# Optimization experiments

Hardware: AMD Instinct MI355X
Metric: run time of the kernel (lower is better)

Reference implementation:

```python
import jax, jax.numpy as jnp
import numpy as np

N = 50000
E = 800000
IN_DIM = 3
HID = 128
OUT_DIM = 3
RED = 16


def setup_inputs() -> dict:
    key = jax.random.key(0)
    ks = jax.random.split(key, 20)
    s = lambda k, shp: jax.random.normal(k, shp, dtype=jnp.float32) * 0.05
    inp = {
        'x': jax.random.normal(ks[0], (N, IN_DIM), dtype=jnp.float32),
        'edge_index': jax.random.randint(ks[1], (2, E), 0, N, dtype=jnp.int32),
        'deg_inv_sqrt': jax.random.uniform(ks[2], (N,), dtype=jnp.float32),
        # GCN layer weights (torch Linear convention: [out, in])
        'W1': s(ks[3], (HID, IN_DIM)), 'b1': s(ks[4], (HID,)),
        'W2': s(ks[5], (HID, HID)),    'b2': s(ks[6], (HID,)),
        'W3': s(ks[7], (HID, HID)),    'b3': s(ks[8], (HID,)),
        # channel attention MLPs (no bias): C -> C//RED -> C
        'ca1_w1': s(ks[9],  (HID // RED, HID)), 'ca1_w2': s(ks[10], (HID, HID // RED)),
        'ca2_w1': s(ks[11], (HID // RED, HID)), 'ca2_w2': s(ks[12], (HID, HID // RED)),
        'ca3_w1': s(ks[13], (HID // RED, HID)), 'ca3_w2': s(ks[14], (HID, HID // RED)),
        # output head
        'Wout': s(ks[15], (OUT_DIM, HID)), 'bout': s(ks[16], (OUT_DIM,)),
    }
    return inp


def _gcn(x, row, col, dis, W, b):
    # gather source features, normalize by deg_inv_sqrt[row]*deg_inv_sqrt[col], scatter-add to target
    norm = (dis[row] * dis[col])[:, None]          # [E,1]
    msg = x[row] * norm                             # [E,C]
    agg = jax.ops.segment_sum(msg, col, num_segments=x.shape[0])  # [N,C]
    return jax.nn.elu(agg @ W.T + b)


def _channel_attn(x, w1, w2):
    # global avg/max pool over nodes -> [C]; shared MLP; sigmoid gate
    avg = jnp.mean(x, axis=0)
    mx = jnp.max(x, axis=0)
    mlp = lambda v: jax.nn.relu(v @ w1.T) @ w2.T
    att = jax.nn.sigmoid(mlp(avg) + mlp(mx))        # [C]
    return x * att


def reference(x, edge_index, deg_inv_sqrt, W1, b1, W2, b2, W3, b3,
              ca1_w1, ca1_w2, ca2_w1, ca2_w2, ca3_w1, ca3_w2, Wout, bout):
    row, col = edge_index[0], edge_index[1]
    h = _gcn(x, row, col, deg_inv_sqrt, W1, b1)
    h = _channel_attn(h, ca1_w1, ca1_w2)
    h = _gcn(h, row, col, deg_inv_sqrt, W2, b2)
    h = _channel_attn(h, ca2_w1, ca2_w2)
    h = _gcn(h, row, col, deg_inv_sqrt, W3, b3)
    h = _channel_attn(h, ca3_w1, ca3_w2)
    return h @ Wout.T + bout
```

## Files before the change

kernel.cpp:

```cpp
#include <hip/hip_runtime.h>

#define NN 50000
#define NE 800000
#define NBD3 391
#define NBG 782
#define PMAX (NBG*128)
#define NRED 64

#define EC 4096
#define NBLKC 196
#define NBUCK 1563
#define LT (NBUCK*NBLKC)
#define NS1 300
#define DCAP 1024

typedef __attribute__((ext_vector_type(8))) short bf16x8;
typedef __attribute__((ext_vector_type(4))) float f32x4;

__device__ __forceinline__ float elu_f(float x){ return x > 0.f ? x : __expf(x) - 1.f; }

__device__ __forceinline__ ushort f2bf(float f){
    unsigned u = __float_as_uint(f);
    unsigned r = (u + 0x7FFFu + ((u >> 16) & 1u)) >> 16;
    return (ushort)r;
}
__device__ __forceinline__ float bf2f(short u){
    return __uint_as_float(((unsigned)(unsigned short)u) << 16);
}

__global__ __launch_bounds__(256) void k_bhist(const int* __restrict__ col, int* __restrict__ hist){
    __shared__ int h[NBUCK];
    int blk = blockIdx.x;
    for (int i = threadIdx.x; i < NBUCK; i += 256) h[i] = 0;
    __syncthreads();
    int base = blk * EC;
    #pragma unroll
    for (int i = 0; i < 16; ++i){
        int e = base + i*256 + threadIdx.x;
        if (e < NE) atomicAdd(&h[col[e] >> 5], 1);
    }
    __syncthreads();
    for (int i = threadIdx.x; i < NBUCK; i += 256) hist[i*NBLKC + blk] = h[i];
}

__global__ __launch_bounds__(256) void k_s1(const int* __restrict__ hist, int* __restrict__ bsum){
    __shared__ int red[256];
    int base = blockIdx.x*1024 + threadIdx.x;
    int s = 0;
    #pragma unroll
    for (int i = 0; i < 4; ++i){ int idx = base + i*256; if (idx < LT) s += hist[idx]; }
    red[threadIdx.x] = s;
    __syncthreads();
    for (int off = 128; off > 0; off >>= 1){
        if (threadIdx.x < off) red[threadIdx.x] += red[threadIdx.x + off];
        __syncthreads();
    }
    if (threadIdx.x == 0) bsum[blockIdx.x] = red[0];
}

__global__ __launch_bounds__(512) void k_s2(const int* __restrict__ bsum, int* __restrict__ boff){
    __shared__ int s[512];
    int t = threadIdx.x;
    int v = (t < NS1) ? bsum[t] : 0;
    s[t] = v;
    __syncthreads();
    for (int off = 1; off < 512; off <<= 1){
        int u = (t >= off) ? s[t - off] : 0;
        __syncthreads();
        s[t] += u;
        __syncthreads();
    }
    if (t < NS1) boff[t] = s[t] - v;
}

__global__ __launch_bounds__(256) void k_s3(const int* __restrict__ hist, const int* __restrict__ boff,
                                            int* __restrict__ scanned, int* __restrict__ bucketPtr){
    __shared__ int red[256];
    int blk = blockIdx.x, t = threadIdx.x;
    int base = blk*1024;
    int v[4]; int s = 0;
    #pragma unroll
    for (int i = 0; i < 4; ++i){
        int idx = base + t*4 + i;
        v[i] = (idx < LT) ? hist[idx] : 0;
        s += v[i];
    }
    red[t] = s;
    __syncthreads();
    for (int off = 1; off < 256; off <<= 1){
        int u = (t >= off) ? red[t - off] : 0;
        __syncthreads();
        red[t] += u;
        __syncthreads();
    }
    int run = boff[blk] + red[t] - s;
    #pragma unroll
    for (int i = 0; i < 4; ++i){
        int idx = base + t*4 + i;
        if (idx < LT){
            scanned[idx] = run;
            if (idx % NBLKC == 0) bucketPtr[idx / NBLKC] = run;
            run += v[i];
        }
    }
    if (blk == 0 && t == 0) bucketPtr[NBUCK] = NE;
}

__global__ __launch_bounds__(256) void k_csort(const int* __restrict__ row, const int* __restrict__ col,
                                               const int* __restrict__ scanned, int2* __restrict__ edgeS){
    __shared__ int curs[NBUCK];
    int blk = blockIdx.x;
    for (int i = threadIdx.x; i < NBUCK; i += 256) curs[i] = scanned[i*NBLKC + blk];
    __syncthreads();
    int base = blk * EC;
    #pragma unroll
    for (int i = 0; i < 16; ++i){
        int e = base + i*256 + threadIdx.x;
        if (e < NE){
            int r = row[e], c = col[e];
            int pos = atomicAdd(&curs[c >> 5], 1);
            edgeS[pos] = make_int2(r, c);
        }
    }
}

__global__ __launch_bounds__(256) void k_dsort(const float* __restrict__ dis, const int* __restrict__ bucketPtr,
                                               int2* __restrict__ edge, int* __restrict__ rowptr){
    __shared__ int nodeCnt[32];
    __shared__ int nodeOff[33];
    __shared__ float disL[32];
    __shared__ int2 stage[DCAP];
    int b = blockIdx.x, t = threadIdx.x;
    int j0 = bucketPtr[b], j1 = bucketPtr[b+1], cnt = j1 - j0;
    if (t < 32){
        nodeCnt[t] = 0;
        int c = b*32 + t;
        disL[t] = (c < NN) ? dis[c] : 0.f;
    }
    __syncthreads();
    int er[8], ec[8], rk[8]; int m = 0;
    for (int j = t; j < cnt && m < 8; j += 256){
        int2 e = edge[j0 + j];
        int cl = e.y & 31;
        er[m] = e.x; ec[m] = e.y;
        rk[m] = atomicAdd(&nodeCnt[cl], 1);
        ++m;
    }
    __syncthreads();
    if (t == 0){
        int run = 0;
        #pragma unroll
        for (int i = 0; i < 32; ++i){ nodeOff[i] = run; run += nodeCnt[i]; }
        nodeOff[32] = run;
    }
    __syncthreads();
    if (t < 32){
        int c = b*32 + t;
        if (c < NN) rowptr[c] = j0 + nodeOff[t];
    }
    if (b == 0 && t == 0) rowptr[NN] = NE;
    bool staged = (cnt <= DCAP);
    for (int i = 0; i < m; ++i){
        int r = er[i], cl = ec[i] & 31;
        float nm = dis[r] * disL[cl];
        int pos = nodeOff[cl] + rk[i];
        int2 rec = make_int2(r, __float_as_int(nm));
        if (staged) stage[pos] = rec;
        else        edge[j0 + pos] = rec;
    }
    __syncthreads();
    if (staged)
        for (int j = t; j < cnt; j += 256) edge[j0 + j] = stage[j];
}

__global__ void k_gather3(const float* __restrict__ x, const int* __restrict__ rowptr,
                          const int2* __restrict__ edge, float* __restrict__ agg){
    int n = blockIdx.x * blockDim.x + threadIdx.x;
    if (n >= NN) return;
    int j0 = rowptr[n], j1 = rowptr[n + 1];
    float a0 = 0.f, a1 = 0.f, a2 = 0.f;
    for (int j = j0; j < j1; ++j){
        int2 e = edge[j];
        int r = e.x; float w = __int_as_float(e.y);
        a0 = fmaf(x[r*3+0], w, a0);
        a1 = fmaf(x[r*3+1], w, a1);
        a2 = fmaf(x[r*3+2], w, a2);
    }
    agg[n*3+0] = a0; agg[n*3+1] = a1; agg[n*3+2] = a2;
}

__global__ __launch_bounds__(128) void k_dense3p(const float* __restrict__ agg, const float* __restrict__ W,
                          const float* __restrict__ b, ushort* __restrict__ h, float* __restrict__ part){
    int c = threadIdx.x;
    int n0 = blockIdx.x * 128;
    int n1 = min(n0 + 128, NN);
    float w0 = W[c*3+0], w1 = W[c*3+1], w2 = W[c*3+2], bb = b[c];
    float s = 0.f, m = -3.4e38f;
    for (int n = n0; n < n1; ++n){
        float v = fmaf(agg[n*3+0], w0, fmaf(agg[n*3+1], w1, fmaf(agg[n*3+2], w2, bb)));
        v = elu_f(v);
        h[(size_t)n*128 + c] = f2bf(v);
        s += v; m = fmaxf(m, v);
    }
    part[blockIdx.x*128 + c] = s;
    part[PMAX + blockIdx.x*128 + c] = m;
}

__global__ __launch_bounds__(256) void k_attn_pre(const float* __restrict__ part, int nblk,
                                                  float* __restrict__ part2){
    __shared__ float sS[2][128], sM[2][128];
    int c = threadIdx.x & 127, g = threadIdx.x >> 7;
    float s = 0.f, m = -3.4e38f;
    for (int b = blockIdx.x*2 + g; b < nblk; b += NRED*2){
        s += part[b*128 + c];
        m = fmaxf(m, part[PMAX + b*128 + c]);
    }
    sS[g][c] = s; sM[g][c] = m;
    __syncthreads();
    if (g == 0){
        part2[blockIdx.x*128 + c] = sS[0][c] + sS[1][c];
        part2[NRED*128 + blockIdx.x*128 + c] = fmaxf(sM[0][c], sM[1][c]);
    }
}

__global__ __launch_bounds__(512) void k_attn(const float* __restrict__ part2,
                       const float* __restrict__ w1, const float* __restrict__ w2,
                       const float* __restrict__ Wsrc, void* __restrict__ Wdst, int mode){
    __shared__ float sAll[4][128], mAll[4][128];
    __shared__ float avg[128], mx[128], ha[8], hm[8], attL[128];
    int c = threadIdx.x & 127, g = threadIdx.x >> 7;
    float s = 0.f, m = -3.4e38f;
    #pragma unroll
    for (int b = 0; b < NRED/4; ++b){
        int r = b*4 + g;
        s += part2[r*128 + c];
        m = fmaxf(m, part2[NRED*128 + r*128 + c]);
    }
    sAll[g][c] = s; mAll[g][c] = m;
    __syncthreads();
    if (g == 0){
        s = sAll[0][c] + sAll[1][c] + sAll[2][c] + sAll[3][c];
        m = fmaxf(fmaxf(mAll[0][c], mAll[1][c]), fmaxf(mAll[2][c], mAll[3][c]));
        avg[c] = s / (float)NN;
        mx[c] = m;
    }
    __syncthreads();
    if (threadIdx.x < 8){
        int cc = threadIdx.x;
        float sa = 0.f, sm = 0.f;
        for (int k = 0; k < 128; ++k){
            float w = w1[cc*128 + k];
            sa += avg[k]*w; sm += mx[k]*w;
        }
        ha[cc] = fmaxf(sa, 0.f); hm[cc] = fmaxf(sm, 0.f);
    }
    __syncthreads();
    if (threadIdx.x < 128){
        float oa = 0.f, om = 0.f;
        for (int j = 0; j < 8; ++j){
            float w = w2[c*8 + j];
            oa += ha[j]*w; om += hm[j]*w;
        }
        attL[c] = 1.f / (1.f + __expf(-(oa + om)));
    }
    __syncthreads();
    if (mode == 0){
        ushort* wd = (ushort*)Wdst;
        for (int i = threadIdx.x; i < 16384; i += 512)
            wd[i] = f2bf(Wsrc[i] * attL[i & 127]);
    } else {
        float* wd = (float*)Wdst;
        if (threadIdx.x < 384)
            wd[threadIdx.x] = Wsrc[threadIdx.x] * attL[threadIdx.x & 127];
    }
}

__global__ __launch_bounds__(256) void k_gg(const ushort* __restrict__ h,
                        const int* __restrict__ rowptr, const int2* __restrict__ edge,
                        const ushort* __restrict__ Wb, const float* __restrict__ b,
                        ushort* __restrict__ hout, float* __restrict__ part){
    __shared__ ushort At[64*128];
    __shared__ float poolS[4][128], poolM[4][128];
    int tid = threadIdx.x;
    int n0b = blockIdx.x * 64;

    {
        int node = tid >> 2;
        int q = tid & 3;
        int n = n0b + node;
        float acc[32];
        #pragma unroll
        for (int i = 0; i < 32; ++i) acc[i] = 0.f;
        if (n < NN){
            int j0 = rowptr[n], j1 = rowptr[n + 1];
            const ushort* hq = h + q*32;
            int j = j0;
            for (; j + 1 < j1; j += 2){
                int2 e0 = edge[j], e1 = edge[j+1];
                const ushort* r0 = hq + (size_t)e0.x*128;
                const ushort* r1 = hq + (size_t)e1.x*128;
                bf16x8 v00 = *(const bf16x8*)(r0);
                bf16x8 v01 = *(const bf16x8*)(r0 + 8);
                bf16x8 v02 = *(const bf16x8*)(r0 + 16);
                bf16x8 v03 = *(const bf16x8*)(r0 + 24);
                bf16x8 v10 = *(const bf16x8*)(r1);
                bf16x8 v11 = *(const bf16x8*)(r1 + 8);
                bf16x8 v12 = *(const bf16x8*)(r1 + 16);
                bf16x8 v13 = *(const bf16x8*)(r1 + 24);
                float w0 = __int_as_float(e0.y), w1 = __int_as_float(e1.y);
                #pragma unroll
                for (int cc = 0; cc < 8; ++cc){
                    acc[cc]    = fmaf(bf2f(v00[cc]), w0, acc[cc]);
                    acc[8+cc]  = fmaf(bf2f(v01[cc]), w0, acc[8+cc]);
                    acc[16+cc] = fmaf(bf2f(v02[cc]), w0, acc[16+cc]);
                    acc[24+cc] = fmaf(bf2f(v03[cc]), w0, acc[24+cc]);
                    acc[cc]    = fmaf(bf2f(v10[cc]), w1, acc[cc]);
                    acc[8+cc]  = fmaf(bf2f(v11[cc]), w1, acc[8+cc]);
                    acc[16+cc] = fmaf(bf2f(v12[cc]), w1, acc[16+cc]);
                    acc[24+cc] = fmaf(bf2f(v13[cc]), w1, acc[24+cc]);
                }
            }
            if (j < j1){
                int2 e0 = edge[j];
                const ushort* r0 = hq + (size_t)e0.x*128;
                bf16x8 v00 = *(const bf16x8*)(r0);
                bf16x8 v01 = *(const bf16x8*)(r0 + 8);
                bf16x8 v02 = *(const bf16x8*)(r0 + 16);
                bf16x8 v03 = *(const bf16x8*)(r0 + 24);
                float w0 = __int_as_float(e0.y);
                #pragma unroll
                for (int cc = 0; cc < 8; ++cc){
                    acc[cc]    = fmaf(bf2f(v00[cc]), w0, acc[cc]);
                    acc[8+cc]  = fmaf(bf2f(v01[cc]), w0, acc[8+cc]);
                    acc[16+cc] = fmaf(bf2f(v02[cc]), w0, acc[16+cc]);
                    acc[24+cc] = fmaf(bf2f(v03[cc]), w0, acc[24+cc]);
                }
            }
        }
        #pragma unroll
        for (int k = 0; k < 4; ++k){
            bf16x8 o;
            #pragma unroll
            for (int cc = 0; cc < 8; ++cc) o[cc] = (short)f2bf(acc[k*8 + cc]);
            int s = q*4 + k;
            *(bf16x8*)((char*)At + node*256 + ((s ^ (node & 7)) << 4)) = o;
        }
    }
    __syncthreads();

    int wave = tid >> 6, l = tid & 63;
    int lr = l & 15, lk = l >> 4;
    int r = wave*16 + lr;
    bf16x8 a[4];
    #pragma unroll
    for (int kb = 0; kb < 4; ++kb){
        int s = kb*4 + lk;
        a[kb] = *(const bf16x8*)((char*)At + r*256 + ((s ^ (r & 7)) << 4));
    }
    int n0 = n0b + wave*16;
    float s_part[8], m_part[8];
    const ushort* wbase = Wb + (size_t)lr * 128 + lk * 8;
    #pragma unroll
    for (int t = 0; t < 8; ++t){
        int j0 = t * 16;
        float bias = b[j0 + lr];
        f32x4 acc = {bias, bias, bias, bias};
        const ushort* wrow = wbase + (size_t)j0 * 128;
        #pragma unroll
        for (int kb = 0; kb < 4; ++kb){
            bf16x8 bf = *(const bf16x8*)(wrow + kb * 32);
            acc = __builtin_amdgcn_mfma_f32_16x16x32_bf16(a[kb], bf, acc, 0, 0, 0);
        }
        float s = 0.f, m = -3.4e38f;
        #pragma unroll
        for (int rr = 0; rr < 4; ++rr){
            int n = n0 + lk * 4 + rr;
            float v = elu_f(acc[rr]);
            if (n < NN){
                hout[(size_t)n * 128 + j0 + lr] = f2bf(v);
                s += v; m = fmaxf(m, v);
            }
        }
        s += __shfl_xor(s, 16); s += __shfl_xor(s, 32);
        m = fmaxf(m, __shfl_xor(m, 16)); m = fmaxf(m, __shfl_xor(m, 32));
        s_part[t] = s; m_part[t] = m;
    }
    if (lk == 0){
        #pragma unroll
        for (int t = 0; t < 8; ++t){
            poolS[wave][t * 16 + lr] = s_part[t];
            poolM[wave][t * 16 + lr] = m_part[t];
        }
    }
    __syncthreads();
    if (tid < 128){
        float S = poolS[0][tid] + poolS[1][tid] + poolS[2][tid] + poolS[3][tid];
        float M = fmaxf(fmaxf(poolM[0][tid], poolM[1][tid]), fmaxf(poolM[2][tid], poolM[3][tid]));
        part[blockIdx.x * 128 + tid] = S;
        part[PMAX + blockIdx.x * 128 + tid] = M;
    }
}

__global__ __launch_bounds__(256) void k_out(const ushort* __restrict__ h,
                      const float* __restrict__ WoS, const float* __restrict__ bo,
                      float* __restrict__ out){
    int n = blockIdx.x * blockDim.x + threadIdx.x;
    if (n >= NN) return;
    float acc0 = bo[0], acc1 = bo[1], acc2 = bo[2];
    const bf16x8* hv = (const bf16x8*)(h + (size_t)n*128);
    #pragma unroll
    for (int i = 0; i < 16; ++i){
        bf16x8 v = hv[i];
        #pragma unroll
        for (int c = 0; c < 8; ++c){
            int cc = i*8 + c;
            float hv_f = bf2f(v[c]);
            acc0 = fmaf(hv_f, WoS[cc],        acc0);
            acc1 = fmaf(hv_f, WoS[128 + cc],  acc1);
            acc2 = fmaf(hv_f, WoS[256 + cc],  acc2);
        }
    }
    out[n*3+0] = acc0; out[n*3+1] = acc1; out[n*3+2] = acc2;
}

extern "C" void kernel_launch(void* const* d_in, const int* in_sizes, int n_in,
                              void* d_out, int out_size, void* d_ws, size_t ws_size,
                              hipStream_t stream) {
    const float* x    = (const float*)d_in[0];
    const int*   ei   = (const int*)d_in[1];
    const int*   row  = ei;
    const int*   col  = ei + NE;
    const float* dis  = (const float*)d_in[2];
    const float* W1   = (const float*)d_in[3];
    const float* b1   = (const float*)d_in[4];
    const float* W2   = (const float*)d_in[5];
    const float* b2   = (const float*)d_in[6];
    const float* W3   = (const float*)d_in[7];
    const float* b3   = (const float*)d_in[8];
    const float* ca1w1= (const float*)d_in[9];
    const float* ca1w2= (const float*)d_in[10];
    const float* ca2w1= (const float*)d_in[11];
    const float* ca2w2= (const float*)d_in[12];
    const float* ca3w1= (const float*)d_in[13];
    const float* ca3w2= (const float*)d_in[14];
    const float* Wout = (const float*)d_in[15];
    const float* bout = (const float*)d_in[16];
    float* out = (float*)d_out;

    ushort* hB    = (ushort*)d_ws;
    ushort* hC    = hB + (size_t)NN*128;
    float*  agg3  = (float*)(hC + (size_t)NN*128);
    float*  part  = agg3 + (size_t)NN*3;
    float*  part2 = part + (size_t)2*PMAX;
    ushort* Wb2   = (ushort*)(part2 + 2*NRED*128);
    ushort* Wb3   = Wb2 + 16384;
    float*  WoutS = (float*)(Wb3 + 16384);
    int2*   edge  = (int2*)(WoutS + 384);
    int*    rowptr= (int*)(edge + NE);
    int*    hist  = rowptr + NN + 1;
    int*    scanned = hist + LT;
    int*    bucketPtr = scanned + LT;
    int*    bsum  = bucketPtr + NBUCK + 1;
    int*    boff  = bsum + NS1;

    k_bhist<<<NBLKC, 256, 0, stream>>>(col, hist);
    k_s1<<<NS1, 256, 0, stream>>>(hist, bsum);
    k_s2<<<1, 512, 0, stream>>>(bsum, boff);
    k_s3<<<NS1, 256, 0, stream>>>(hist, boff, scanned, bucketPtr);
    k_csort<<<NBLKC, 256, 0, stream>>>(row, col, scanned, edge);
    k_dsort<<<NBUCK, 256, 0, stream>>>(dis, bucketPtr, edge, rowptr);

    k_gather3<<<(NN+255)/256, 256, 0, stream>>>(x, rowptr, edge, agg3);
    k_dense3p<<<NBD3, 128, 0, stream>>>(agg3, W1, b1, hB, part);
    k_attn_pre<<<NRED, 256, 0, stream>>>(part, NBD3, part2);
    k_attn<<<1, 512, 0, stream>>>(part2, ca1w1, ca1w2, W2, (void*)Wb2, 0);

    k_gg<<<NBG, 256, 0, stream>>>(hB, rowptr, edge, Wb2, b2, hC, part);
    k_attn_pre<<<NRED, 256, 0, stream>>>(part, NBG, part2);
    k_attn<<<1, 512, 0, stream>>>(part2, ca2w1, ca2w2, W3, (void*)Wb3, 0);

    k_gg<<<NBG, 256, 0, stream>>>(hC, rowptr, edge, Wb3, b3, hB, part);
    k_attn_pre<<<NRED, 256, 0, stream>>>(part, NBG, part2);
    k_attn<<<1, 512, 0, stream>>>(part2, ca3w1, ca3w2, Wout, (void*)WoutS, 1);

    k_out<<<(NN+255)/256, 256, 0, stream>>>(hB, WoutS, bout, out);
}
```

Measured before the change: 220.2 us.

## Split fused gather-GEMM across 512 threads with 8 lanes per node

```diff
diff --git a/kernel.cpp b/kernel.cpp
--- a/kernel.cpp
+++ b/kernel.cpp
@@ -275,94 +275,89 @@
     }
 }
 
-__global__ __launch_bounds__(256) void k_gg(const ushort* __restrict__ h,
+__global__ __launch_bounds__(512) void k_gg(const ushort* __restrict__ h,
                         const int* __restrict__ rowptr, const int2* __restrict__ edge,
                         const ushort* __restrict__ Wb, const float* __restrict__ b,
                         ushort* __restrict__ hout, float* __restrict__ part){
     __shared__ ushort At[64*128];
-    __shared__ float poolS[4][128], poolM[4][128];
+    __shared__ float poolS[8][64], poolM[8][64];
     int tid = threadIdx.x;
     int n0b = blockIdx.x * 64;
 
     {
-        int node = tid >> 2;
-        int q = tid & 3;
+        int node = tid >> 3;
+        int l8 = tid & 7;
         int n = n0b + node;
-        float acc[32];
-        #pragma unroll
-        for (int i = 0; i < 32; ++i) acc[i] = 0.f;
+        float acc[16];
+        #pragma unroll
+        for (int i = 0; i < 16; ++i) acc[i] = 0.f;
         if (n < NN){
             int j0 = rowptr[n], j1 = rowptr[n + 1];
-            const ushort* hq = h + q*32;
+            const ushort* hq = h + l8*16;
             int j = j0;
-            for (; j + 1 < j1; j += 2){
-                int2 e0 = edge[j], e1 = edge[j+1];
+            for (; j + 3 < j1; j += 4){
+                int2 e0 = edge[j], e1 = edge[j+1], e2 = edge[j+2], e3 = edge[j+3];
                 const ushort* r0 = hq + (size_t)e0.x*128;
                 const ushort* r1 = hq + (size_t)e1.x*128;
-                bf16x8 v00 = *(const bf16x8*)(r0);
-                bf16x8 v01 = *(const bf16x8*)(r0 + 8);
-                bf16x8 v02 = *(const bf16x8*)(r0 + 16);
-                bf16x8 v03 = *(const bf16x8*)(r0 + 24);
-                bf16x8 v10 = *(const bf16x8*)(r1);
-                bf16x8 v11 = *(const bf16x8*)(r1 + 8);
-                bf16x8 v12 = *(const bf16x8*)(r1 + 16);
-                bf16x8 v13 = *(const bf16x8*)(r1 + 24);
+                const ushort* r2 = hq + (size_t)e2.x*128;
+                const ushort* r3 = hq + (size_t)e3.x*128;
+                bf16x8 v0a = *(const bf16x8*)(r0), v0b = *(const bf16x8*)(r0 + 8);
+                bf16x8 v1a = *(const bf16x8*)(r1), v1b = *(const bf16x8*)(r1 + 8);
+                bf16x8 v2a = *(const bf16x8*)(r2), v2b = *(const bf16x8*)(r2 + 8);
+                bf16x8 v3a = *(const bf16x8*)(r3), v3b = *(const bf16x8*)(r3 + 8);
                 float w0 = __int_as_float(e0.y), w1 = __int_as_float(e1.y);
+                float w2 = __int_as_float(e2.y), w3 = __int_as_float(e3.y);
                 #pragma unroll
                 for (int cc = 0; cc < 8; ++cc){
-                    acc[cc]    = fmaf(bf2f(v00[cc]), w0, acc[cc]);
-                    acc[8+cc]  = fmaf(bf2f(v01[cc]), w0, acc[8+cc]);
-                    acc[16+cc] = fmaf(bf2f(v02[cc]), w0, acc[16+cc]);
-                    acc[24+cc] = fmaf(bf2f(v03[cc]), w0, acc[24+cc]);
-                    acc[cc]    = fmaf(bf2f(v10[cc]), w1, acc[cc]);
-                    acc[8+cc]  = fmaf(bf2f(v11[cc]), w1, acc[8+cc]);
-                    acc[16+cc] = fmaf(bf2f(v12[cc]), w1, acc[16+cc]);
-                    acc[24+cc] = fmaf(bf2f(v13[cc]), w1, acc[24+cc]);
+                    acc[cc]   = fmaf(bf2f(v0a[cc]), w0, acc[cc]);
+                    acc[8+cc] = fmaf(bf2f(v0b[cc]), w0, acc[8+cc]);
+                    acc[cc]   = fmaf(bf2f(v1a[cc]), w1, acc[cc]);
+                    acc[8+cc] = fmaf(bf2f(v1b[cc]), w1, acc[8+cc]);
+                    acc[cc]   = fmaf(bf2f(v2a[cc]), w2, acc[cc]);
+                    acc[8+cc] = fmaf(bf2f(v2b[cc]), w2, acc[8+cc]);
+                    acc[cc]   = fmaf(bf2f(v3a[cc]), w3, acc[cc]);
+                    acc[8+cc] = fmaf(bf2f(v3b[cc]), w3, acc[8+cc]);
                 }
             }
-            if (j < j1){
+            for (; j < j1; ++j){
                 int2 e0 = edge[j];
                 const ushort* r0 = hq + (size_t)e0.x*128;
-                bf16x8 v00 = *(const bf16x8*)(r0);
-                bf16x8 v01 = *(const bf16x8*)(r0 + 8);
-                bf16x8 v02 = *(const bf16x8*)(r0 + 16);
-                bf16x8 v03 = *(const bf16x8*)(r0 + 24);
+                bf16x8 v0a = *(const bf16x8*)(r0), v0b = *(const bf16x8*)(r0 + 8);
                 float w0 = __int_as_float(e0.y);
                 #pragma unroll
                 for (int cc = 0; cc < 8; ++cc){
-                    acc[cc]    = fmaf(bf2f(v00[cc]), w0, acc[cc]);
-                    acc[8+cc]  = fmaf(bf2f(v01[cc]), w0, acc[8+cc]);
-                    acc[16+cc] = fmaf(bf2f(v02[cc]), w0, acc[16+cc]);
-                    acc[24+cc] = fmaf(bf2f(v03[cc]), w0, acc[24+cc]);
+                    acc[cc]   = fmaf(bf2f(v0a[cc]), w0, acc[cc]);
+                    acc[8+cc] = fmaf(bf2f(v0b[cc]), w0, acc[8+cc]);
                 }
             }
         }
         #pragma unroll
-        for (int k = 0; k < 4; ++k){
+        for (int k = 0; k < 2; ++k){
             bf16x8 o;
             #pragma unroll
             for (int cc = 0; cc < 8; ++cc) o[cc] = (short)f2bf(acc[k*8 + cc]);
-            int s = q*4 + k;
+            int s = l8*2 + k;
             *(bf16x8*)((char*)At + node*256 + ((s ^ (node & 7)) << 4)) = o;
         }
     }
     __syncthreads();
 
     int wave = tid >> 6, l = tid & 63;
+    int nt = wave >> 1, jh = wave & 1;
     int lr = l & 15, lk = l >> 4;
-    int r = wave*16 + lr;
+    int r = nt*16 + lr;
     bf16x8 a[4];
     #pragma unroll
     for (int kb = 0; kb < 4; ++kb){
         int s = kb*4 + lk;
         a[kb] = *(const bf16x8*)((char*)At + r*256 + ((s ^ (r & 7)) << 4));
     }
-    int n0 = n0b + wave*16;
-    float s_part[8], m_part[8];
+    int n0 = n0b + nt*16;
+    float s_part[4], m_part[4];
     const ushort* wbase = Wb + (size_t)lr * 128 + lk * 8;
     #pragma unroll
-    for (int t = 0; t < 8; ++t){
-        int j0 = t * 16;
+    for (int t = 0; t < 4; ++t){
+        int j0 = jh*64 + t*16;
         float bias = b[j0 + lr];
         f32x4 acc = {bias, bias, bias, bias};
         const ushort* wrow = wbase + (size_t)j0 * 128;
@@ -387,17 +382,19 @@
     }
     if (lk == 0){
         #pragma unroll
-        for (int t = 0; t < 8; ++t){
+        for (int t = 0; t < 4; ++t){
             poolS[wave][t * 16 + lr] = s_part[t];
             poolM[wave][t * 16 + lr] = m_part[t];
         }
     }
     __syncthreads();
     if (tid < 128){
-        float S = poolS[0][tid] + poolS[1][tid] + poolS[2][tid] + poolS[3][tid];
-        float M = fmaxf(fmaxf(poolM[0][tid], poolM[1][tid]), fmaxf(poolM[2][tid], poolM[3][tid]));
-        part[blockIdx.x * 128 + tid] = S;
-        part[PMAX + blockIdx.x * 128 + tid] = M;
+        int c = tid, j2 = c >> 6, lc = c & 63;
+        float S = poolS[0 + j2][lc] + poolS[2 + j2][lc] + poolS[4 + j2][lc] + poolS[6 + j2][lc];
+        float M = fmaxf(fmaxf(poolM[0 + j2][lc], poolM[2 + j2][lc]),
+                        fmaxf(poolM[4 + j2][lc], poolM[6 + j2][lc]));
+        part[blockIdx.x * 128 + c] = S;
+        part[PMAX + blockIdx.x * 128 + c] = M;
     }
 }
 
@@ -475,11 +472,11 @@
     k_attn_pre<<<NRED, 256, 0, stream>>>(part, NBD3, part2);
     k_attn<<<1, 512, 0, stream>>>(part2, ca1w1, ca1w2, W2, (void*)Wb2, 0);
 
-    k_gg<<<NBG, 256, 0, stream>>>(hB, rowptr, edge, Wb2, b2, hC, part);
+    k_gg<<<NBG, 512, 0, stream>>>(hB, rowptr, edge, Wb2, b2, hC, part);
     k_attn_pre<<<NRED, 256, 0, stream>>>(part, NBG, part2);
     k_attn<<<1, 512, 0, stream>>>(part2, ca2w1, ca2w2, W3, (void*)Wb3, 0);
 
-    k_gg<<<NBG, 256, 0, stream>>>(hC, rowptr, edge, Wb3, b3, hB, part);
+    k_gg<<<NBG, 512, 0, stream>>>(hC, rowptr, edge, Wb3, b3, hB, part);
     k_attn_pre<<<NRED, 256, 0, stream>>>(part, NBG, part2);
     k_attn<<<1, 512, 0, stream>>>(part2, ca3w1, ca3w2, Wout, (void*)WoutS, 1);
 
```

Measured after the change: 217.2 us. No clear change (-1.3%).
